# Optimization experiments

Hardware: AMD Instinct MI355X
Metric: run time of the kernel (lower is better)

## Reference

```python
import jax, jax.numpy as jnp
import numpy as np

N = 100_000          # nodes
E = 3_200_000        # edges (avg degree 32)
DIMS = [6, 20, 15, 10, 5, 2]


def setup_inputs() -> dict:
    key = jax.random.key(0)
    ks = jax.random.split(key, 3 + 2 * 5)
    inp = {
        "x": jax.random.normal(ks[0], (N, DIMS[0]), jnp.float32),
        "edge_index": jax.random.randint(ks[1], (2, E), 0, N, jnp.int32),
        "edge_weight": jax.random.uniform(ks[2], (E,), jnp.float32),
    }
    for i in range(5):
        din, dout = DIMS[i], DIMS[i + 1]
        s = 1.0 / np.sqrt(din)
        inp[f"w_rel{i}"] = jax.random.normal(ks[3 + 2 * i], (din, dout), jnp.float32) * s
        inp[f"b_rel{i}"] = jnp.zeros((dout,), jnp.float32)
        inp[f"w_root{i}"] = jax.random.normal(ks[4 + 2 * i], (din, dout), jnp.float32) * s
    return inp


def _graph_conv(x, src, dst, w, W_rel, b_rel, W_root):
    # PyG GraphConv: lin_rel(scatter_add(w_e * x_src)) + lin_root(x)
    msg = x[src] * w[:, None]                                  # [E, din]
    agg = jax.ops.segment_sum(msg, dst, num_segments=N)        # [N, din]
    return agg @ W_rel + b_rel + x @ W_root                    # [N, dout]


def reference(x, edge_index, edge_weight,
              w_rel0, b_rel0, w_root0,
              w_rel1, b_rel1, w_root1,
              w_rel2, b_rel2, w_root2,
              w_rel3, b_rel3, w_root3,
              w_rel4, b_rel4, w_root4):
    src, dst = edge_index[0], edge_index[1]
    layers = [
        (w_rel0, b_rel0, w_root0),
        (w_rel1, b_rel1, w_root1),
        (w_rel2, b_rel2, w_root2),
        (w_rel3, b_rel3, w_root3),
        (w_rel4, b_rel4, w_root4),
    ]
    for W_rel, b_rel, W_root in layers:
        x = jax.nn.relu(_graph_conv(x, src, dst, edge_weight, W_rel, b_rel, W_root))
    return jax.nn.softmax(x, axis=1)
```

## Files before the change

kernel.cpp:

```cpp
#include <hip/hip_runtime.h>
#include <hip/hip_fp16.h>
#include <stdint.h>

#define N_NODES 100000
#define N_EDGES 3200000
#define BN      64
#define NB      1563
#define NCH_H   1024
#define CH_H    (N_EDGES / NCH_H)
#define CPL     (NCH_H / 64)
#define NCH_S   256
#define CH_S    (N_EDGES / NCH_S)
#define BS1     1024
#define S1_IT   ((CH_S + BS1 - 1) / BS1)
#define S2_CAP  2560
#define BLOCK   256
#define W_SCALE 32767.0f
#define W_INV   (1.0f / 32767.0f)

__global__ void pad_x_kernel(const float* __restrict__ x, __half* __restrict__ xpad) {
    int i = blockIdx.x * blockDim.x + threadIdx.x;
    if (i < N_NODES) {
        const float* xr = x + (size_t)i * 6;
        __half2 h[4];
        h[0] = __halves2half2(__float2half(xr[0]), __float2half(xr[1]));
        h[1] = __halves2half2(__float2half(xr[2]), __float2half(xr[3]));
        h[2] = __halves2half2(__float2half(xr[4]), __float2half(xr[5]));
        h[3] = __halves2half2(__float2half(0.f),   __float2half(0.f));
        *(uint4*)(xpad + (size_t)i * 8) = *(uint4*)h;
    }
}

__global__ void hist_kernel(const int* __restrict__ dst, int* __restrict__ hist_g) {
    __shared__ int h[NB];
    for (int b = threadIdx.x; b < NB; b += BLOCK) h[b] = 0;
    __syncthreads();
    const int c  = blockIdx.x;
    const int k0 = c * CH_H;
    for (int k = threadIdx.x; k < CH_H; k += BLOCK)
        atomicAdd(&h[dst[k0 + k] >> 6], 1);
    __syncthreads();
    for (int b = threadIdx.x; b < NB; b += BLOCK)
        hist_g[c * NB + b] = h[b];
}

__global__ void chunkscan_kernel(const int* __restrict__ hist_g,
                                 int* __restrict__ off_g, int* __restrict__ tot) {
    int w    = (blockIdx.x * blockDim.x + threadIdx.x) >> 6;
    int lane = threadIdx.x & 63;
    if (w >= NB) return;
    int v[CPL];
    int ls = 0;
    const int cbase = lane * CPL;
    #pragma unroll
    for (int i = 0; i < CPL; ++i) { v[i] = hist_g[(cbase + i) * NB + w]; ls += v[i]; }
    int run = ls;
    #pragma unroll
    for (int d = 1; d < 64; d <<= 1) {
        int u = __shfl_up(run, d);
        if (lane >= d) run += u;
    }
    int acc = run - ls;
    #pragma unroll
    for (int i = 0; i < CPL; ++i) { off_g[(cbase + i) * NB + w] = acc; acc += v[i]; }
    if (lane == 63) tot[w] = acc;
}

#define SCAN_T   1024
#define SCAN_PER 2
__global__ void scan_kernel(const int* __restrict__ cnt, int* __restrict__ bstart) {
    __shared__ int part[SCAN_T];
    int t = threadIdx.x;
    int local[SCAN_PER];
    int s = 0;
    #pragma unroll
    for (int i = 0; i < SCAN_PER; ++i) {
        int idx = t * SCAN_PER + i;
        int v = (idx < NB) ? cnt[idx] : 0;
        local[i] = s;
        s += v;
    }
    part[t] = s;
    __syncthreads();
    for (int off = 1; off < SCAN_T; off <<= 1) {
        int v = (t >= off) ? part[t - off] : 0;
        __syncthreads();
        part[t] += v;
        __syncthreads();
    }
    int excl = part[t] - s;
    #pragma unroll
    for (int i = 0; i < SCAN_PER; ++i) {
        int idx = t * SCAN_PER + i;
        if (idx < NB) bstart[idx] = excl + local[i];
    }
}

__global__ void __launch_bounds__(BS1)
scatter1_kernel(const int* __restrict__ src, const int* __restrict__ dst,
                const float* __restrict__ w,
                const int* __restrict__ bstart, const int* __restrict__ off_g,
                uint2* __restrict__ rec1) {
    __shared__ uint32_t stage[CH_S];
    __shared__ int h[NB];
    __shared__ int delta[NB];
    __shared__ int wtot[BS1 / 64];

    const int c  = blockIdx.x;
    const int k0 = c * CH_S;
    const int t  = threadIdx.x;

    for (int b = t; b < NB; b += BS1) h[b] = 0;
    __syncthreads();
    int dstv[S1_IT];
    int nit = 0;
    for (int k = t; k < CH_S; k += BS1, ++nit) {
        int d = dst[k0 + k];
        dstv[nit] = d;
        atomicAdd(&h[d >> 6], 1);
    }
    __syncthreads();

    {
        const int base = t * 2;
        int v[2], ls = 0;
        #pragma unroll
        for (int i = 0; i < 2; ++i) {
            int idx = base + i;
            v[i] = (idx < NB) ? h[idx] : 0;
            ls += v[i];
        }
        int lane = t & 63, wv = t >> 6;
        int run = ls;
        #pragma unroll
        for (int d = 1; d < 64; d <<= 1) {
            int u = __shfl_up(run, d);
            if (lane >= d) run += u;
        }
        if (lane == 63) wtot[wv] = run;
        __syncthreads();
        int wexcl = 0;
        for (int i = 0; i < wv; ++i) wexcl += wtot[i];
        int excl = wexcl + run - ls;
        #pragma unroll
        for (int i = 0; i < 2; ++i) {
            int idx = base + i;
            if (idx < NB) {
                int gb = bstart[idx] + off_g[(size_t)(4 * c) * NB + idx];
                h[idx]     = excl;
                delta[idx] = gb - excl;
                excl += v[i];
            }
        }
    }
    __syncthreads();

    nit = 0;
    for (int k = t; k < CH_S; k += BS1, ++nit) {
        int d = dstv[nit];
        int b = d >> 6;
        int pos = atomicAdd(&h[b], 1);
        stage[pos] = (uint32_t)k | ((uint32_t)(d & 63) << 14) | ((uint32_t)b << 20);
    }
    __syncthreads();

    for (int i = t; i < CH_S; i += BS1) {
        uint32_t sv = stage[i];
        int le = sv & 0x3FFF;
        int dl = (sv >> 14) & 0x3F;
        int b  = sv >> 20;
        int e  = k0 + le;
        uint2 r;
        r.x = (uint32_t)src[e] | ((uint32_t)dl << 17);
        r.y = __float_as_uint(w[e]);
        rec1[delta[b] + i] = r;
    }
}

__global__ void scatter2_kernel(const uint2* __restrict__ rec1,
                                const int* __restrict__ bstart, const int* __restrict__ tot,
                                uint32_t* __restrict__ rec2,
                                int* __restrict__ row_start, int* __restrict__ cnt) {
    __shared__ int h[BN];
    __shared__ int cur[BN];
    __shared__ uint32_t stage[S2_CAP];
    const int b  = blockIdx.x;
    const int s0 = bstart[b];
    const int n  = tot[b];
    if (threadIdx.x < BN) h[threadIdx.x] = 0;
    __syncthreads();
    for (int k = threadIdx.x; k < n; k += BLOCK)
        atomicAdd(&h[rec1[s0 + k].x >> 17], 1);
    __syncthreads();
    if (threadIdx.x < BN) {
        int v = h[threadIdx.x];
        int run = v;
        #pragma unroll
        for (int d = 1; d < 64; d <<= 1) {
            int u = __shfl_up(run, d);
            if (threadIdx.x >= d) run += u;
        }
        int excl = run - v;
        cur[threadIdx.x] = excl;
        int node = b * BN + threadIdx.x;
        if (node < N_NODES) { row_start[node] = s0 + excl; cnt[node] = v; }
    }
    __syncthreads();
    for (int k = threadIdx.x; k < n; k += BLOCK) {
        uint2 r = rec1[s0 + k];
        int dl = (int)(r.x >> 17);
        float wv = __uint_as_float(r.y);
        uint32_t w15 = (uint32_t)__float2uint_rn(wv * W_SCALE);
        uint32_t r2 = (r.x & 0x1FFFF) | (w15 << 17);
        int pos = atomicAdd(&cur[dl], 1);
        if (pos < S2_CAP) stage[pos] = r2;
        else              rec2[s0 + pos] = r2;
    }
    __syncthreads();
    for (int i = threadIdx.x; i < n && i < S2_CAP; i += BLOCK)
        rec2[s0 + i] = stage[i];
}

__global__ void layer0_kernel(const __half* __restrict__ xpad,
                              const uint32_t* __restrict__ rec,
                              const int* __restrict__ row_start, const int* __restrict__ cnt,
                              const float* __restrict__ wrel, const float* __restrict__ brel,
                              const float* __restrict__ wroot,
                              float* __restrict__ out) {
    __shared__ float s_wrel[6 * 20];
    __shared__ float s_wroot[6 * 20];
    __shared__ float s_b[20];
    for (int t = threadIdx.x; t < 120; t += BLOCK) {
        s_wrel[t]  = wrel[t];
        s_wroot[t] = wroot[t];
    }
    if (threadIdx.x < 20) s_b[threadIdx.x] = brel[threadIdx.x];
    __syncthreads();

    int t = blockIdx.x * blockDim.x + threadIdx.x;
    int node = t >> 3;
    int q    = t & 7;
    if (node >= N_NODES) return;

    float agg[6] = {0.f, 0.f, 0.f, 0.f, 0.f, 0.f};
    const int s = row_start[node];
    const int e = s + cnt[node];
    for (int k = s + q; k < e; k += 8) {
        uint32_t r = rec[k];
        float w = (float)(r >> 17) * W_INV;
        uint4 raw = *(const uint4*)(xpad + (size_t)(r & 0x1FFFF) * 8);
        const __half2* h = (const __half2*)&raw;
        agg[0] += w * __low2float(h[0]);  agg[1] += w * __high2float(h[0]);
        agg[2] += w * __low2float(h[1]);  agg[3] += w * __high2float(h[1]);
        agg[4] += w * __low2float(h[2]);  agg[5] += w * __high2float(h[2]);
    }
    #pragma unroll
    for (int i = 0; i < 6; ++i) {
        agg[i] += __shfl_xor(agg[i], 1);
        agg[i] += __shfl_xor(agg[i], 2);
        agg[i] += __shfl_xor(agg[i], 4);
    }
    uint4 raws = *(const uint4*)(xpad + (size_t)node * 8);
    const __half2* hs = (const __half2*)&raws;
    float xv[6] = { __low2float(hs[0]), __high2float(hs[0]),
                    __low2float(hs[1]), __high2float(hs[1]),
                    __low2float(hs[2]), __high2float(hs[2]) };

    const int j0 = q * 3;
    #pragma unroll
    for (int jj = 0; jj < 3; ++jj) {
        int j = j0 + jj;
        if (j < 20) {
            float o = s_b[j];
            #pragma unroll
            for (int i = 0; i < 6; ++i)
                o += agg[i] * s_wrel[i * 20 + j] + xv[i] * s_wroot[i * 20 + j];
            out[(size_t)node * 20 + j] = fmaxf(o, 0.f);
        }
    }
}

template<int DIN, int DOUT, int SPH>
__global__ void dense_kernel(const float* __restrict__ xin,
                             const float* __restrict__ wrel, const float* __restrict__ brel,
                             const float* __restrict__ wroot,
                             __half* __restrict__ p, float* __restrict__ oinit) {
    __shared__ float s_wrel[DIN * DOUT];
    __shared__ float s_wroot[DIN * DOUT];
    __shared__ float s_b[DOUT];
    for (int t = threadIdx.x; t < DIN * DOUT; t += BLOCK) {
        s_wrel[t]  = wrel[t];
        s_wroot[t] = wroot[t];
    }
    if (threadIdx.x < DOUT) s_b[threadIdx.x] = brel[threadIdx.x];
    __syncthreads();

    int node = blockIdx.x * blockDim.x + threadIdx.x;
    if (node >= N_NODES) return;

    float xv[DIN];
    #pragma unroll
    for (int i = 0; i < DIN; ++i) xv[i] = xin[(size_t)node * DIN + i];

    float pv[DOUT], ov[DOUT];
    #pragma unroll
    for (int j = 0; j < DOUT; ++j) { pv[j] = 0.f; ov[j] = s_b[j]; }
    #pragma unroll
    for (int i = 0; i < DIN; ++i) {
        float xi = xv[i];
        #pragma unroll
        for (int j = 0; j < DOUT; ++j) {
            pv[j] += xi * s_wrel[i * DOUT + j];
            ov[j] += xi * s_wroot[i * DOUT + j];
        }
    }
    __half2* prow = (__half2*)(p + (size_t)node * SPH);
    #pragma unroll
    for (int jj = 0; jj < SPH / 2; ++jj) {
        float a = (2 * jj     < DOUT) ? pv[2 * jj]     : 0.f;
        float b = (2 * jj + 1 < DOUT) ? pv[2 * jj + 1] : 0.f;
        prow[jj] = __halves2half2(__float2half(a), __float2half(b));
    }
    #pragma unroll
    for (int j = 0; j < DOUT; ++j) oinit[(size_t)node * DOUT + j] = ov[j];
}

template<int DOUT, int SPH, bool LAST>
__global__ void gather_kernel(const __half* __restrict__ p, const float* __restrict__ oinit,
                              const uint32_t* __restrict__ rec,
                              const int* __restrict__ row_start, const int* __restrict__ cnt,
                              float* __restrict__ out) {
    int t = blockIdx.x * blockDim.x + threadIdx.x;
    int node = t >> 3;
    int q    = t & 7;
    if (node >= N_NODES) return;

    float af[SPH];
    #pragma unroll
    for (int i = 0; i < SPH; ++i) af[i] = 0.f;

    const int s = row_start[node];
    const int e = s + cnt[node];
    for (int k = s + q; k < e; k += 8) {
        uint32_t r = rec[k];
        float w = (float)(r >> 17) * W_INV;
        const __half* ps = p + (size_t)(r & 0x1FFFF) * SPH;
        if constexpr (SPH >= 8) {
            #pragma unroll
            for (int v = 0; v < SPH / 8; ++v) {
                uint4 raw = ((const uint4*)ps)[v];
                const __half2* h = (const __half2*)&raw;
                #pragma unroll
                for (int jj = 0; jj < 4; ++jj) {
                    af[v * 8 + 2 * jj]     += w * __low2float(h[jj]);
                    af[v * 8 + 2 * jj + 1] += w * __high2float(h[jj]);
                }
            }
        } else {
            uint32_t raw = *(const uint32_t*)ps;
            __half2 h = *(const __half2*)&raw;
            af[0] += w * __low2float(h);
            af[1] += w * __high2float(h);
        }
    }
    #pragma unroll
    for (int i = 0; i < SPH; ++i) {
        af[i] += __shfl_xor(af[i], 1);
        af[i] += __shfl_xor(af[i], 2);
        af[i] += __shfl_xor(af[i], 4);
    }

    if (LAST) {
        if (q == 0) {
            float o0 = af[0] + oinit[(size_t)node * 2 + 0];
            float o1 = af[1] + oinit[(size_t)node * 2 + 1];
            float m = fmaxf(o0, o1);
            float e0 = __expf(o0 - m), e1 = __expf(o1 - m);
            float inv = 1.f / (e0 + e1);
            out[(size_t)node * 2 + 0] = e0 * inv;
            out[(size_t)node * 2 + 1] = e1 * inv;
        }
    } else {
        constexpr int PER = (DOUT + 7) / 8;
        #pragma unroll
        for (int jj = 0; jj < PER; ++jj) {
            int j = q * PER + jj;
            if (j < DOUT)
                out[(size_t)node * DOUT + j] =
                    fmaxf(af[j] + oinit[(size_t)node * DOUT + j], 0.f);
        }
    }
}


extern "C" void kernel_launch(void* const* d_in, const int* in_sizes, int n_in,
                              void* d_out, int out_size, void* d_ws, size_t ws_size,
                              hipStream_t stream) {
    const float* x  = (const float*)d_in[0];
    const int*   ei = (const int*)d_in[1];
    const float* ew = (const float*)d_in[2];
    const float* wrel[5]  = { (const float*)d_in[3], (const float*)d_in[6],
                              (const float*)d_in[9], (const float*)d_in[12],
                              (const float*)d_in[15] };
    const float* brel[5]  = { (const float*)d_in[4], (const float*)d_in[7],
                              (const float*)d_in[10], (const float*)d_in[13],
                              (const float*)d_in[16] };
    const float* wroot[5] = { (const float*)d_in[5], (const float*)d_in[8],
                              (const float*)d_in[11], (const float*)d_in[14],
                              (const float*)d_in[17] };

    char* ws = (char*)d_ws;
    size_t off = 0;
    auto alloc = [&](size_t bytes) -> void* {
        void* ptr = ws + off;
        off += (bytes + 255) & ~(size_t)255;
        return ptr;
    };
    char*     regionA   = (char*)alloc((size_t)N_EDGES * 8);
    uint2*    rec1      = (uint2*)regionA;
    __half*   pbuf      = (__half*)regionA;
    float*    oinit     = (float*)(regionA + (size_t)8 * 1024 * 1024);
    uint32_t* rec2      = (uint32_t*)alloc((size_t)N_EDGES * 4);
    __half*   xpad      = (__half*)alloc((size_t)N_NODES * 8 * 2);
    char*     regionB   = (char*)alloc((size_t)14 * 1024 * 1024);
    int*      hist_g    = (int*)regionB;
    int*      off_g     = (int*)(regionB + (size_t)NCH_H * NB * 4);
    float*    fA        = (float*)regionB;
    float*    fB        = (float*)(regionB + (size_t)8 * 1024 * 1024);
    int*      tot       = (int*)alloc((size_t)NB * 4);
    int*      bstart    = (int*)alloc((size_t)NB * 4);
    int*      row_start = (int*)alloc((size_t)N_NODES * 4);
    int*      cntb      = (int*)alloc((size_t)N_NODES * 4);

    const int* srcv = ei;
    const int* dstv = ei + N_EDGES;

    const int gN  = (N_NODES + BLOCK - 1) / BLOCK;
    const int gN8 = (8 * N_NODES + BLOCK - 1) / BLOCK;

    pad_x_kernel    <<<gN, BLOCK, 0, stream>>>(x, xpad);
    hist_kernel     <<<NCH_H, BLOCK, 0, stream>>>(dstv, hist_g);
    chunkscan_kernel<<<(NB + 3) / 4, BLOCK, 0, stream>>>(hist_g, off_g, tot);
    scan_kernel     <<<1, SCAN_T, 0, stream>>>(tot, bstart);
    scatter1_kernel <<<NCH_S, BS1, 0, stream>>>(srcv, dstv, ew, bstart, off_g, rec1);
    scatter2_kernel <<<NB, BLOCK, 0, stream>>>(rec1, bstart, tot, rec2, row_start, cntb);

    layer0_kernel<<<gN8, BLOCK, 0, stream>>>(xpad, rec2, row_start, cntb,
                                             wrel[0], brel[0], wroot[0], fA);
    dense_kernel<20, 15, 16><<<gN, BLOCK, 0, stream>>>(fA, wrel[1], brel[1], wroot[1], pbuf, oinit);
    gather_kernel<15, 16, false><<<gN8, BLOCK, 0, stream>>>(pbuf, oinit, rec2, row_start, cntb, fB);
    dense_kernel<15, 10, 16><<<gN, BLOCK, 0, stream>>>(fB, wrel[2], brel[2], wroot[2], pbuf, oinit);
    gather_kernel<10, 16, false><<<gN8, BLOCK, 0, stream>>>(pbuf, oinit, rec2, row_start, cntb, fA);
    dense_kernel<10, 5, 8><<<gN, BLOCK, 0, stream>>>(fA, wrel[3], brel[3], wroot[3], pbuf, oinit);
    gather_kernel<5, 8, false><<<gN8, BLOCK, 0, stream>>>(pbuf, oinit, rec2, row_start, cntb, fB);
    dense_kernel<5, 2, 2><<<gN, BLOCK, 0, stream>>>(fB, wrel[4], brel[4], wroot[4], pbuf, oinit);
    gather_kernel<2, 2, true><<<gN8, BLOCK, 0, stream>>>(pbuf, oinit, rec2, row_start, cntb, (float*)d_out);
}
```

Baseline: 343.0 us.

## Fuse dense projections into gather epilogues and split scatter records

Each layer's dense transform (project with W_rel into fp16 p and W_root plus bias into oinit) now runs in the epilogue of the previous gather kernel, and layer0 also computes layer 1's projections. This removes four dense kernel launches and the write and re-read of intermediate float activations. The x padding is folded into hist_kernel, and scatter1 now writes a packed 32-bit record plus a separate byte for the local destination, so scatter2 reads less data and no longer converts weights. In exchange every thread in a node group recomputes all of ov redundantly, extra shared-memory weight loads are added per block, and the node bounds checks were removed.

After: 330.5 us. -3.6%, faster.

```diff
diff --git a/kernel.cpp b/kernel.cpp
--- a/kernel.cpp
+++ b/kernel.cpp
@@ -9,6 +9,7 @@
 #define NCH_H   1024
 #define CH_H    (N_EDGES / NCH_H)
 #define CPL     (NCH_H / 64)
+#define PAD_PER 98
 #define NCH_S   256
 #define CH_S    (N_EDGES / NCH_S)
 #define BS1     1024
@@ -18,22 +19,22 @@
 #define W_SCALE 32767.0f
 #define W_INV   (1.0f / 32767.0f)
 
-__global__ void pad_x_kernel(const float* __restrict__ x, __half* __restrict__ xpad) {
-    int i = blockIdx.x * blockDim.x + threadIdx.x;
-    if (i < N_NODES) {
-        const float* xr = x + (size_t)i * 6;
-        __half2 h[4];
-        h[0] = __halves2half2(__float2half(xr[0]), __float2half(xr[1]));
-        h[1] = __halves2half2(__float2half(xr[2]), __float2half(xr[3]));
-        h[2] = __halves2half2(__float2half(xr[4]), __float2half(xr[5]));
-        h[3] = __halves2half2(__float2half(0.f),   __float2half(0.f));
-        *(uint4*)(xpad + (size_t)i * 8) = *(uint4*)h;
-    }
-}
-
-__global__ void hist_kernel(const int* __restrict__ dst, int* __restrict__ hist_g) {
+__global__ void hist_kernel(const int* __restrict__ dst, int* __restrict__ hist_g,
+                            const float* __restrict__ x, __half* __restrict__ xpad) {
     __shared__ int h[NB];
     for (int b = threadIdx.x; b < NB; b += BLOCK) h[b] = 0;
+    {
+        int i = blockIdx.x * PAD_PER + threadIdx.x;
+        if (threadIdx.x < PAD_PER && i < N_NODES) {
+            const float* xr = x + (size_t)i * 6;
+            __half2 hh[4];
+            hh[0] = __halves2half2(__float2half(xr[0]), __float2half(xr[1]));
+            hh[1] = __halves2half2(__float2half(xr[2]), __float2half(xr[3]));
+            hh[2] = __halves2half2(__float2half(xr[4]), __float2half(xr[5]));
+            hh[3] = __halves2half2(__float2half(0.f),   __float2half(0.f));
+            *(uint4*)(xpad + (size_t)i * 8) = *(uint4*)hh;
+        }
+    }
     __syncthreads();
     const int c  = blockIdx.x;
     const int k0 = c * CH_H;
@@ -100,7 +101,7 @@
 scatter1_kernel(const int* __restrict__ src, const int* __restrict__ dst,
                 const float* __restrict__ w,
                 const int* __restrict__ bstart, const int* __restrict__ off_g,
-                uint2* __restrict__ rec1) {
+                uint32_t* __restrict__ recA, uint8_t* __restrict__ recD) {
     __shared__ uint32_t stage[CH_S];
     __shared__ int h[NB];
     __shared__ int delta[NB];
@@ -170,14 +171,15 @@
         int dl = (sv >> 14) & 0x3F;
         int b  = sv >> 20;
         int e  = k0 + le;
-        uint2 r;
-        r.x = (uint32_t)src[e] | ((uint32_t)dl << 17);
-        r.y = __float_as_uint(w[e]);
-        rec1[delta[b] + i] = r;
-    }
-}
-
-__global__ void scatter2_kernel(const uint2* __restrict__ rec1,
+        uint32_t w15 = (uint32_t)__float2uint_rn(w[e] * W_SCALE);
+        int pos = delta[b] + i;
+        recA[pos] = (uint32_t)src[e] | (w15 << 17);
+        recD[pos] = (uint8_t)dl;
+    }
+}
+
+__global__ void scatter2_kernel(const uint32_t* __restrict__ recA,
+                                const uint8_t* __restrict__ recD,
                                 const int* __restrict__ bstart, const int* __restrict__ tot,
                                 uint32_t* __restrict__ rec2,
                                 int* __restrict__ row_start, int* __restrict__ cnt) {
@@ -190,7 +192,7 @@
     if (threadIdx.x < BN) h[threadIdx.x] = 0;
     __syncthreads();
     for (int k = threadIdx.x; k < n; k += BLOCK)
-        atomicAdd(&h[rec1[s0 + k].x >> 17], 1);
+        atomicAdd(&h[recD[s0 + k]], 1);
     __syncthreads();
     if (threadIdx.x < BN) {
         int v = h[threadIdx.x];
@@ -207,14 +209,11 @@
     }
     __syncthreads();
     for (int k = threadIdx.x; k < n; k += BLOCK) {
-        uint2 r = rec1[s0 + k];
-        int dl = (int)(r.x >> 17);
-        float wv = __uint_as_float(r.y);
-        uint32_t w15 = (uint32_t)__float2uint_rn(wv * W_SCALE);
-        uint32_t r2 = (r.x & 0x1FFFF) | (w15 << 17);
+        uint32_t ra = recA[s0 + k];
+        int dl = recD[s0 + k];
         int pos = atomicAdd(&cur[dl], 1);
-        if (pos < S2_CAP) stage[pos] = r2;
-        else              rec2[s0 + pos] = r2;
+        if (pos < S2_CAP) stage[pos] = ra;
+        else              rec2[s0 + pos] = ra;
     }
     __syncthreads();
     for (int i = threadIdx.x; i < n && i < S2_CAP; i += BLOCK)
@@ -224,23 +223,28 @@
 __global__ void layer0_kernel(const __half* __restrict__ xpad,
                               const uint32_t* __restrict__ rec,
                               const int* __restrict__ row_start, const int* __restrict__ cnt,
-                              const float* __restrict__ wrel, const float* __restrict__ brel,
-                              const float* __restrict__ wroot,
-                              float* __restrict__ out) {
-    __shared__ float s_wrel[6 * 20];
-    __shared__ float s_wroot[6 * 20];
-    __shared__ float s_b[20];
+                              const float* __restrict__ wrel0, const float* __restrict__ brel0,
+                              const float* __restrict__ wroot0,
+                              const float* __restrict__ wrel1, const float* __restrict__ brel1,
+                              const float* __restrict__ wroot1,
+                              __half* __restrict__ pn, float* __restrict__ oinitn) {
+    __shared__ float s_wrel0[6 * 20], s_wroot0[6 * 20], s_b0[20];
+    __shared__ float s_wrel1[20 * 15], s_wroot1[20 * 15], s_b1[15];
     for (int t = threadIdx.x; t < 120; t += BLOCK) {
-        s_wrel[t]  = wrel[t];
-        s_wroot[t] = wroot[t];
-    }
-    if (threadIdx.x < 20) s_b[threadIdx.x] = brel[threadIdx.x];
+        s_wrel0[t]  = wrel0[t];
+        s_wroot0[t] = wroot0[t];
+    }
+    for (int t = threadIdx.x; t < 300; t += BLOCK) {
+        s_wrel1[t]  = wrel1[t];
+        s_wroot1[t] = wroot1[t];
+    }
+    if (threadIdx.x < 20) s_b0[threadIdx.x] = brel0[threadIdx.x];
+    else if (threadIdx.x >= 32 && threadIdx.x < 47) s_b1[threadIdx.x - 32] = brel1[threadIdx.x - 32];
     __syncthreads();
 
     int t = blockIdx.x * blockDim.x + threadIdx.x;
     int node = t >> 3;
     int q    = t & 7;
-    if (node >= N_NODES) return;
 
     float agg[6] = {0.f, 0.f, 0.f, 0.f, 0.f, 0.f};
     const int s = row_start[node];
@@ -266,74 +270,66 @@
                     __low2float(hs[1]), __high2float(hs[1]),
                     __low2float(hs[2]), __high2float(hs[2]) };
 
-    const int j0 = q * 3;
-    #pragma unroll
-    for (int jj = 0; jj < 3; ++jj) {
-        int j = j0 + jj;
-        if (j < 20) {
-            float o = s_b[j];
+    float ov[20];
+    #pragma unroll
+    for (int j = 0; j < 20; ++j) {
+        float o = s_b0[j];
+        #pragma unroll
+        for (int i = 0; i < 6; ++i)
+            o += agg[i] * s_wrel0[i * 20 + j] + xv[i] * s_wroot0[i * 20 + j];
+        ov[j] = fmaxf(o, 0.f);
+    }
+
+    {
+        float pk[2] = {0.f, 0.f};
+        #pragma unroll
+        for (int kk = 0; kk < 2; ++kk) {
+            int k = 2 * q + kk;
+            if (k < 15) {
+                float sacc = 0.f;
+                #pragma unroll
+                for (int j = 0; j < 20; ++j) sacc += ov[j] * s_wrel1[j * 15 + k];
+                pk[kk] = sacc;
+            }
+        }
+        ((__half2*)(pn + (size_t)node * 16))[q] =
+            __halves2half2(__float2half(pk[0]), __float2half(pk[1]));
+    }
+    #pragma unroll
+    for (int kk = 0; kk < 2; ++kk) {
+        int k = q + kk * 8;
+        if (k < 15) {
+            float sacc = s_b1[k];
             #pragma unroll
-            for (int i = 0; i < 6; ++i)
-                o += agg[i] * s_wrel[i * 20 + j] + xv[i] * s_wroot[i * 20 + j];
-            out[(size_t)node * 20 + j] = fmaxf(o, 0.f);
-        }
-    }
-}
-
-template<int DIN, int DOUT, int SPH>
-__global__ void dense_kernel(const float* __restrict__ xin,
-                             const float* __restrict__ wrel, const float* __restrict__ brel,
-                             const float* __restrict__ wroot,
-                             __half* __restrict__ p, float* __restrict__ oinit) {
-    __shared__ float s_wrel[DIN * DOUT];
-    __shared__ float s_wroot[DIN * DOUT];
-    __shared__ float s_b[DOUT];
-    for (int t = threadIdx.x; t < DIN * DOUT; t += BLOCK) {
-        s_wrel[t]  = wrel[t];
-        s_wroot[t] = wroot[t];
-    }
-    if (threadIdx.x < DOUT) s_b[threadIdx.x] = brel[threadIdx.x];
-    __syncthreads();
-
-    int node = blockIdx.x * blockDim.x + threadIdx.x;
-    if (node >= N_NODES) return;
-
-    float xv[DIN];
-    #pragma unroll
-    for (int i = 0; i < DIN; ++i) xv[i] = xin[(size_t)node * DIN + i];
-
-    float pv[DOUT], ov[DOUT];
-    #pragma unroll
-    for (int j = 0; j < DOUT; ++j) { pv[j] = 0.f; ov[j] = s_b[j]; }
-    #pragma unroll
-    for (int i = 0; i < DIN; ++i) {
-        float xi = xv[i];
-        #pragma unroll
-        for (int j = 0; j < DOUT; ++j) {
-            pv[j] += xi * s_wrel[i * DOUT + j];
-            ov[j] += xi * s_wroot[i * DOUT + j];
-        }
-    }
-    __half2* prow = (__half2*)(p + (size_t)node * SPH);
-    #pragma unroll
-    for (int jj = 0; jj < SPH / 2; ++jj) {
-        float a = (2 * jj     < DOUT) ? pv[2 * jj]     : 0.f;
-        float b = (2 * jj + 1 < DOUT) ? pv[2 * jj + 1] : 0.f;
-        prow[jj] = __halves2half2(__float2half(a), __float2half(b));
-    }
-    #pragma unroll
-    for (int j = 0; j < DOUT; ++j) oinit[(size_t)node * DOUT + j] = ov[j];
-}
-
-template<int DOUT, int SPH, bool LAST>
+            for (int j = 0; j < 20; ++j) sacc += ov[j] * s_wroot1[j * 15 + k];
+            oinitn[(size_t)node * 15 + k] = sacc;
+        }
+    }
+}
+
+template<int DOUT, int SPH, int NDOUT, int NSPH, bool LAST>
 __global__ void gather_kernel(const __half* __restrict__ p, const float* __restrict__ oinit,
                               const uint32_t* __restrict__ rec,
                               const int* __restrict__ row_start, const int* __restrict__ cnt,
+                              const float* __restrict__ wrel_n, const float* __restrict__ brel_n,
+                              const float* __restrict__ wroot_n,
+                              __half* __restrict__ pn, float* __restrict__ oinitn,
                               float* __restrict__ out) {
+    __shared__ float s_wrel[LAST ? 1 : DOUT * NDOUT];
+    __shared__ float s_wroot[LAST ? 1 : DOUT * NDOUT];
+    __shared__ float s_b[LAST ? 1 : (NDOUT > 0 ? NDOUT : 1)];
+    if constexpr (!LAST) {
+        for (int t = threadIdx.x; t < DOUT * NDOUT; t += BLOCK) {
+            s_wrel[t]  = wrel_n[t];
+            s_wroot[t] = wroot_n[t];
+        }
+        if (threadIdx.x < NDOUT) s_b[threadIdx.x] = brel_n[threadIdx.x];
+        __syncthreads();
+    }
+
     int t = blockIdx.x * blockDim.x + threadIdx.x;
     int node = t >> 3;
     int q    = t & 7;
-    if (node >= N_NODES) return;
 
     float af[SPH];
     #pragma unroll
@@ -370,7 +366,7 @@
         af[i] += __shfl_xor(af[i], 4);
     }
 
-    if (LAST) {
+    if constexpr (LAST) {
         if (q == 0) {
             float o0 = af[0] + oinit[(size_t)node * 2 + 0];
             float o1 = af[1] + oinit[(size_t)node * 2 + 1];
@@ -381,13 +377,35 @@
             out[(size_t)node * 2 + 1] = e1 * inv;
         }
     } else {
-        constexpr int PER = (DOUT + 7) / 8;
-        #pragma unroll
-        for (int jj = 0; jj < PER; ++jj) {
-            int j = q * PER + jj;
-            if (j < DOUT)
-                out[(size_t)node * DOUT + j] =
-                    fmaxf(af[j] + oinit[(size_t)node * DOUT + j], 0.f);
+        float ov[DOUT];
+        #pragma unroll
+        for (int j = 0; j < DOUT; ++j)
+            ov[j] = fmaxf(af[j] + oinit[(size_t)node * DOUT + j], 0.f);
+
+        if (q < NSPH / 2) {
+            float pk[2] = {0.f, 0.f};
+            #pragma unroll
+            for (int kk = 0; kk < 2; ++kk) {
+                int k = 2 * q + kk;
+                if (k < NDOUT) {
+                    float sacc = 0.f;
+                    #pragma unroll
+                    for (int j = 0; j < DOUT; ++j) sacc += ov[j] * s_wrel[j * NDOUT + k];
+                    pk[kk] = sacc;
+                }
+            }
+            ((__half2*)(pn + (size_t)node * NSPH))[q] =
+                __halves2half2(__float2half(pk[0]), __float2half(pk[1]));
+        }
+        #pragma unroll
+        for (int kk = 0; kk < 2; ++kk) {
+            int k = q + kk * 8;
+            if (k < NDOUT) {
+                float sacc = s_b[k];
+                #pragma unroll
+                for (int j = 0; j < DOUT; ++j) sacc += ov[j] * s_wroot[j * NDOUT + k];
+                oinitn[(size_t)node * NDOUT + k] = sacc;
+            }
         }
     }
 }
@@ -416,43 +434,45 @@
         off += (bytes + 255) & ~(size_t)255;
         return ptr;
     };
-    char*     regionA   = (char*)alloc((size_t)N_EDGES * 8);
-    uint2*    rec1      = (uint2*)regionA;
-    __half*   pbuf      = (__half*)regionA;
-    float*    oinit     = (float*)(regionA + (size_t)8 * 1024 * 1024);
+    uint32_t* recA      = (uint32_t*)alloc((size_t)N_EDGES * 4);
+    uint8_t*  recD      = (uint8_t*)alloc((size_t)N_EDGES);
     uint32_t* rec2      = (uint32_t*)alloc((size_t)N_EDGES * 4);
     __half*   xpad      = (__half*)alloc((size_t)N_NODES * 8 * 2);
-    char*     regionB   = (char*)alloc((size_t)14 * 1024 * 1024);
+    char*     regionB   = (char*)alloc((size_t)19 * 1024 * 1024);
     int*      hist_g    = (int*)regionB;
     int*      off_g     = (int*)(regionB + (size_t)NCH_H * NB * 4);
-    float*    fA        = (float*)regionB;
-    float*    fB        = (float*)(regionB + (size_t)8 * 1024 * 1024);
+    __half*   pA        = (__half*)regionB;
+    __half*   pB        = (__half*)(regionB + (size_t)4 * 1024 * 1024);
+    float*    oA        = (float*)(regionB + (size_t)8 * 1024 * 1024);
+    float*    oB        = (float*)(regionB + (size_t)14 * 1024 * 1024);
     int*      tot       = (int*)alloc((size_t)NB * 4);
     int*      bstart    = (int*)alloc((size_t)NB * 4);
     int*      row_start = (int*)alloc((size_t)N_NODES * 4);
     int*      cntb      = (int*)alloc((size_t)N_NODES * 4);
+    float*    oB2       = (float*)alloc((size_t)N_NODES * 15 * 4);
+    oB = oB2;
 
     const int* srcv = ei;
     const int* dstv = ei + N_EDGES;
 
-    const int gN  = (N_NODES + BLOCK - 1) / BLOCK;
     const int gN8 = (8 * N_NODES + BLOCK - 1) / BLOCK;
 
-    pad_x_kernel    <<<gN, BLOCK, 0, stream>>>(x, xpad);
-    hist_kernel     <<<NCH_H, BLOCK, 0, stream>>>(dstv, hist_g);
+    hist_kernel     <<<NCH_H, BLOCK, 0, stream>>>(dstv, hist_g, x, xpad);
     chunkscan_kernel<<<(NB + 3) / 4, BLOCK, 0, stream>>>(hist_g, off_g, tot);
     scan_kernel     <<<1, SCAN_T, 0, stream>>>(tot, bstart);
-    scatter1_kernel <<<NCH_S, BS1, 0, stream>>>(srcv, dstv, ew, bstart, off_g, rec1);
-    scatter2_kernel <<<NB, BLOCK, 0, stream>>>(rec1, bstart, tot, rec2, row_start, cntb);
+    scatter1_kernel <<<NCH_S, BS1, 0, stream>>>(srcv, dstv, ew, bstart, off_g, recA, recD);
+    scatter2_kernel <<<NB, BLOCK, 0, stream>>>(recA, recD, bstart, tot, rec2, row_start, cntb);
 
     layer0_kernel<<<gN8, BLOCK, 0, stream>>>(xpad, rec2, row_start, cntb,
-                                             wrel[0], brel[0], wroot[0], fA);
-    dense_kernel<20, 15, 16><<<gN, BLOCK, 0, stream>>>(fA, wrel[1], brel[1], wroot[1], pbuf, oinit);
-    gather_kernel<15, 16, false><<<gN8, BLOCK, 0, stream>>>(pbuf, oinit, rec2, row_start, cntb, fB);
-    dense_kernel<15, 10, 16><<<gN, BLOCK, 0, stream>>>(fB, wrel[2], brel[2], wroot[2], pbuf, oinit);
-    gather_kernel<10, 16, false><<<gN8, BLOCK, 0, stream>>>(pbuf, oinit, rec2, row_start, cntb, fA);
-    dense_kernel<10, 5, 8><<<gN, BLOCK, 0, stream>>>(fA, wrel[3], brel[3], wroot[3], pbuf, oinit);
-    gather_kernel<5, 8, false><<<gN8, BLOCK, 0, stream>>>(pbuf, oinit, rec2, row_start, cntb, fB);
-    dense_kernel<5, 2, 2><<<gN, BLOCK, 0, stream>>>(fB, wrel[4], brel[4], wroot[4], pbuf, oinit);
-    gather_kernel<2, 2, true><<<gN8, BLOCK, 0, stream>>>(pbuf, oinit, rec2, row_start, cntb, (float*)d_out);
-}
+                                             wrel[0], brel[0], wroot[0],
+                                             wrel[1], brel[1], wroot[1], pA, oA);
+    gather_kernel<15, 16, 10, 16, false><<<gN8, BLOCK, 0, stream>>>(
+        pA, oA, rec2, row_start, cntb, wrel[2], brel[2], wroot[2], pB, oB, nullptr);
+    gather_kernel<10, 16, 5, 8, false><<<gN8, BLOCK, 0, stream>>>(
+        pB, oB, rec2, row_start, cntb, wrel[3], brel[3], wroot[3], pA, oA, nullptr);
+    gather_kernel<5, 8, 2, 2, false><<<gN8, BLOCK, 0, stream>>>(
+        pA, oA, rec2, row_start, cntb, wrel[4], brel[4], wroot[4], pB, oB, nullptr);
+    gather_kernel<2, 2, 0, 0, true><<<gN8, BLOCK, 0, stream>>>(
+        pB, oB, rec2, row_start, cntb, nullptr, nullptr, nullptr,
+        nullptr, nullptr, (float*)d_out);
+}
```
